# Kernel optimization log

Measured on AMD Instinct MI355X. Metric: run time of the kernel, lower is better.

## Reference

```python
import jax, jax.numpy as jnp
import numpy as np

N_NODES = 50000
N_EDGES = 800000
F_IN = 64
F_HID = 64
K = 3


def _cheb_norm(edge_index, edge_weight, n):
    # PyG ChebConv sym normalization with lambda_max=2: Lhat = -D^{-1/2} A D^{-1/2}
    # (diagonal of Lhat is exactly 0, so self-loop terms vanish)
    row, col = edge_index[0], edge_index[1]
    deg = jax.ops.segment_sum(edge_weight, row, num_segments=n)
    dis = jnp.where(deg > 0, jax.lax.rsqrt(jnp.where(deg > 0, deg, 1.0)), 0.0)
    return -dis[row] * edge_weight * dis[col]


def _prop(x, row, col, norm, n):
    # out[i] = sum_{e: col[e]=i} norm[e] * x[row[e]]
    return jax.ops.segment_sum(x[row] * norm[:, None], col, num_segments=n)


def _cheb_conv(x, W, b, row, col, norm, n):
    # ChebConv K=3: Tx0=x, Tx1=Lhat x, Tx2=2 Lhat Tx1 - Tx0
    tx0 = x
    tx1 = _prop(x, row, col, norm, n)
    tx2 = 2.0 * _prop(tx1, row, col, norm, n) - tx0
    return tx0 @ W[0] + tx1 @ W[1] + tx2 @ W[2] + b


def setup_inputs() -> dict:
    key = jax.random.key(0)
    ks = jax.random.split(key, 20)
    inp = {
        "x": jax.random.normal(ks[0], (N_NODES, F_IN), dtype=jnp.float32),
        "edge_index": jax.random.randint(ks[1], (2, N_EDGES), 0, N_NODES, dtype=jnp.int32),
        "edge_weight": jax.random.uniform(ks[2], (N_EDGES,), dtype=jnp.float32),
    }
    # 6 ChebConvs: x->gate (F_IN->F_HID) and h->gate (F_HID->F_HID) for z, r, h
    names_in = [("Wxz", "bxz", F_IN), ("Whz", "bhz", F_HID), ("Wxr", "bxr", F_IN),
                ("Whr", "bhr", F_HID), ("Wxh", "bxh", F_IN), ("Whh", "bhh", F_HID)]
    for i, (wn, bn, fin) in enumerate(names_in):
        scale = 1.0 / np.sqrt(fin)
        inp[wn] = jax.random.normal(ks[3 + i], (K, fin, F_HID), dtype=jnp.float32) * scale
        inp[bn] = jnp.zeros((F_HID,), dtype=jnp.float32)
    inp["Wlin"] = jax.random.normal(ks[12], (F_HID, 2), dtype=jnp.float32) * (1.0 / np.sqrt(F_HID))
    inp["blin"] = jnp.zeros((2,), dtype=jnp.float32)
    return inp


def reference(x, edge_index, edge_weight, Wxz, bxz, Whz, bhz, Wxr, bxr, Whr, bhr,
              Wxh, bxh, Whh, bhh, Wlin, blin):
    n = x.shape[0]
    row, col = edge_index[0], edge_index[1]
    norm = _cheb_norm(edge_index, edge_weight, n)
    h0 = jnp.zeros((n, F_HID), dtype=x.dtype)
    # GConvGRU single step (initial hidden state = 0)
    z = jax.nn.sigmoid(_cheb_conv(x, Wxz, bxz, row, col, norm, n)
                       + _cheb_conv(h0, Whz, bhz, row, col, norm, n))
    r = jax.nn.sigmoid(_cheb_conv(x, Wxr, bxr, row, col, norm, n)
                       + _cheb_conv(h0, Whr, bhr, row, col, norm, n))
    h_tilde = jnp.tanh(_cheb_conv(x, Wxh, bxh, row, col, norm, n)
                       + _cheb_conv(h0 * r, Whh, bhh, row, col, norm, n))
    h = z * h0 + (1.0 - z) * h_tilde
    # head: dropout in eval mode (identity) -> tanh -> linear -> sigmoid
    return jax.nn.sigmoid(jnp.tanh(h) @ Wlin + blin)
```

## Files before the change

kernel.cpp:

```cpp
#include <hip/hip_runtime.h>
#include <hip/hip_bf16.h>

#define N_NODES 50000
#define N_EDGES 800000
#define NB1 400
#define CH  2000
#define NBKT 196
#define CAP 8192
#define SORT_MAX 6144

typedef unsigned short ushort_t;
typedef unsigned long long u64;
typedef __attribute__((ext_vector_type(8))) short bf16x8;
typedef __attribute__((ext_vector_type(4))) float f32x4;

constexpr int GCUR_O  = 0;
constexpr int DIS_O   = 512;
constexpr int OFF_O   = 50512;
constexpr int CSLOT_O = 100544;
constexpr int RSLOT_O = 3311808;
constexpr int RW_O    = 4917440;
constexpr int ABUF_O  = 6517440;
constexpr int PBUF_O  = 11317440;
constexpr int XS_O    = 11329728;
constexpr int T1S_O   = RSLOT_O;

__device__ __forceinline__ ushort_t f32_to_bf16(float f) {
    unsigned u = __float_as_uint(f);
    u += 0x7fffu + ((u >> 16) & 1u);
    return (ushort_t)(u >> 16);
}
__device__ __forceinline__ float bflo(unsigned u) { return __uint_as_float(u << 16); }
__device__ __forceinline__ float bfhi(unsigned u) { return __uint_as_float(u & 0xffff0000u); }
__device__ __forceinline__ unsigned packbf2(float a, float b) {
    return (unsigned)f32_to_bf16(a) | ((unsigned)f32_to_bf16(b) << 16);
}
__device__ __forceinline__ float fsigmoid(float x) { return 1.f / (1.f + __expf(-x)); }
__device__ __forceinline__ float ftanh(float x) {
    x = fminf(15.f, fmaxf(-15.f, x));
    float e = __expf(2.f * x);
    return (e - 1.f) / (e + 1.f);
}

__global__ __launch_bounds__(512) void k1(
    const int* __restrict__ ei, const float* __restrict__ ew,
    const float* __restrict__ x, const float* __restrict__ Wxz,
    const float* __restrict__ Wxh, unsigned* __restrict__ gcur,
    u64* __restrict__ cslot, unsigned* __restrict__ rslot,
    unsigned* __restrict__ abuf, ushort_t* __restrict__ pbuf) {
    int bid = blockIdx.x, t = threadIdx.x;
    if (bid < NB1) {
        __shared__ unsigned colbuf[CH], rowbuf[CH];
        __shared__ unsigned hc[256], hr[256], bc[256], br[256];
        if (t < 256) { hc[t] = 0; hr[t] = 0; }
        __syncthreads();
        int e0 = bid * CH;
        for (int i = t; i < CH; i += 512) {
            unsigned r = (unsigned)ei[e0 + i];
            unsigned c = (unsigned)ei[N_EDGES + e0 + i];
            rowbuf[i] = r;
            colbuf[i] = c;
            atomicAdd(&hc[c >> 8], 1u);
            atomicAdd(&hr[r >> 8], 1u);
        }
        __syncthreads();
        if (t < NBKT) {
            bc[t] = atomicAdd(&gcur[t], hc[t]);
            br[t] = atomicAdd(&gcur[256 + t], hr[t]);
        }
        __syncthreads();
        if (t < 256) { hc[t] = 0; hr[t] = 0; }
        __syncthreads();
        for (int i = t; i < CH; i += 512) {
            unsigned c = colbuf[i];
            unsigned r = rowbuf[i];
            unsigned w = __float_as_uint(ew[e0 + i]);
            unsigned dc = c >> 8;
            unsigned pc = bc[dc] + atomicAdd(&hc[dc], 1u);
            if (pc < CAP)
                cslot[dc * CAP + pc] = ((u64)w << 32) | ((c & 255u) << 16) | (r & 0xFFFFu);
            unsigned dr = r >> 8;
            unsigned pr = br[dr] + atomicAdd(&hr[dr], 1u);
            if (pr < CAP) rslot[dr * CAP + pr] = (w & 0xFFFFFF00u) | (r & 255u);
        }
    } else if (bid < NB1 + 98) {
        int n0 = (bid - NB1) * 512;
        for (int idx = t; idx < 512 * 32; idx += 512) {
            int n = n0 + (idx >> 5);
            if (n < N_NODES) {
                int q = idx & 31;
                float2 xv = ((const float2*)x)[n * 32 + q];
                abuf[n * 96 + q] = packbf2(xv.x, xv.y);
            }
        }
    } else {
        for (int idx = t; idx < 24576; idx += 512) {
            int k = idx >> 7, n = idx & 127;
            float v = (n < 64) ? Wxz[k * 64 + n] : Wxh[k * 64 + (n - 64)];
            int c = n >> 4, s = k >> 5, l = (((k >> 3) & 3) << 4) | (n & 15), j = k & 7;
            pbuf[((c * 6 + s) * 64 + l) * 8 + j] = f32_to_bf16(v);
        }
    }
}

__global__ __launch_bounds__(512) void k2(
    const float* __restrict__ x, const unsigned* __restrict__ gcur,
    const u64* __restrict__ cslot, const unsigned* __restrict__ rslot,
    float* __restrict__ dis, int* __restrict__ off,
    u64* __restrict__ rw, unsigned* __restrict__ xs) {
    int bid = blockIdx.x, t = threadIdx.x;
    __shared__ unsigned rawA[SORT_MAX], rawB[SORT_MAX];
    __shared__ unsigned hist[256], hsc[256], cur[256], gs[256];
    __shared__ float facc[256];

    if (bid < NBKT) {
        if (t < 256) {
            gs[t] = (t < NBKT) ? gcur[t] : 0u;
            hist[t] = 0;
        }
        __syncthreads();
        for (int o = 1; o < 256; o <<= 1) {
            unsigned v = (t < 256 && t >= o) ? gs[t - o] : 0u;
            __syncthreads();
            if (t < 256) gs[t] += v;
            __syncthreads();
        }
        unsigned szb = gcur[bid];
        unsigned sz = min(szb, (unsigned)SORT_MAX);
        unsigned base = gs[bid] - szb;
        for (unsigned i = t; i < sz; i += 512) {
            u64 v = cslot[bid * CAP + i];
            unsigned lo = (unsigned)v;
            rawA[i] = lo;
            rawB[i] = (unsigned)(v >> 32);
            atomicAdd(&hist[(lo >> 16) & 255u], 1u);
        }
        __syncthreads();
        unsigned h0 = (t < 256) ? hist[t] : 0u;
        if (t < 256) hsc[t] = h0;
        __syncthreads();
        for (int o = 1; o < 256; o <<= 1) {
            unsigned v = (t < 256 && t >= o) ? hsc[t - o] : 0u;
            __syncthreads();
            if (t < 256) hsc[t] += v;
            __syncthreads();
        }
        if (t < 256) {
            hsc[t] -= h0;
            cur[t] = 0u;
            int c = bid * 256 + t;
            if (c <= N_NODES) off[c] = (int)(base + hsc[t]);
        }
        __syncthreads();
        for (unsigned i = t; i < sz; i += 512) {
            unsigned lo = rawA[i];
            unsigned d = (lo >> 16) & 255u;
            unsigned p = hsc[d] + atomicAdd(&cur[d], 1u);
            rw[base + p] = ((u64)rawB[i] << 32) | (lo & 0xFFFFu);
        }
    } else {
        int b = bid - NBKT;
        if (t < 256) facc[t] = 0.f;
        __syncthreads();
        unsigned szr = min(gcur[256 + b], (unsigned)CAP);
        for (unsigned i = t; i < szr; i += 512) {
            unsigned v = rslot[b * CAP + i];
            atomicAdd(&facc[v & 255u], __uint_as_float(v & 0xFFFFFF00u));
        }
        __syncthreads();
        if (t < 256) {
            float d = facc[t];
            float r = d > 0.f ? rsqrtf(d) : 0.f;
            facc[t] = r;
            int n = b * 256 + t;
            if (n < N_NODES) dis[n] = r;
        }
        __syncthreads();
        for (int idx = t; idx < 8192; idx += 512) {
            int nl = idx >> 5, q = idx & 31;
            int n = b * 256 + nl;
            if (n < N_NODES) {
                float2 xv = ((const float2*)x)[n * 32 + q];
                float r = facc[nl];
                xs[n * 32 + q] = packbf2(r * xv.x, r * xv.y);
            }
        }
    }
}

__global__ __launch_bounds__(256) void k_prop(
    const int* __restrict__ off, const u64* __restrict__ rw,
    const unsigned* __restrict__ xsrc, const float* __restrict__ dis,
    const float* __restrict__ xf, unsigned* __restrict__ abuf,
    unsigned* __restrict__ t1s, int mode) {
    int node = (blockIdx.x * 256 + threadIdx.x) >> 6;
    if (node >= N_NODES) return;
    int lane = threadIdx.x & 63, h = lane >> 5, q = lane & 31;
    int b = off[node], end = off[node + 1];
    float di = dis[node];
    float acc0 = 0.f, acc1 = 0.f;
    for (; b + 7 < end; b += 8) {
        u64 v0 = rw[b + h], v1 = rw[b + h + 2], v2 = rw[b + h + 4], v3 = rw[b + h + 6];
        unsigned r0 = (unsigned)v0 & 0xFFFFu, r1 = (unsigned)v1 & 0xFFFFu;
        unsigned r2 = (unsigned)v2 & 0xFFFFu, r3 = (unsigned)v3 & 0xFFFFu;
        float a0 = __uint_as_float((unsigned)(v0 >> 32));
        float a1 = __uint_as_float((unsigned)(v1 >> 32));
        float a2 = __uint_as_float((unsigned)(v2 >> 32));
        float a3 = __uint_as_float((unsigned)(v3 >> 32));
        unsigned u0 = xsrc[r0 * 32 + q], u1 = xsrc[r1 * 32 + q];
        unsigned u2 = xsrc[r2 * 32 + q], u3 = xsrc[r3 * 32 + q];
        acc0 += a0 * bflo(u0) + a1 * bflo(u1) + a2 * bflo(u2) + a3 * bflo(u3);
        acc1 += a0 * bfhi(u0) + a1 * bfhi(u1) + a2 * bfhi(u2) + a3 * bfhi(u3);
    }
    for (; b + 1 < end; b += 2) {
        u64 v = rw[b + h];
        unsigned r = (unsigned)v & 0xFFFFu;
        float a = __uint_as_float((unsigned)(v >> 32));
        unsigned u = xsrc[r * 32 + q];
        acc0 += a * bflo(u); acc1 += a * bfhi(u);
    }
    if (b < end && h == 0) {
        u64 v = rw[b];
        unsigned r = (unsigned)v & 0xFFFFu;
        float a = __uint_as_float((unsigned)(v >> 32));
        unsigned u = xsrc[r * 32 + q];
        acc0 += a * bflo(u); acc1 += a * bfhi(u);
    }
    acc0 += __shfl_xor(acc0, 32, 64);
    acc1 += __shfl_xor(acc1, 32, 64);
    if (h == 0) {
        float t0 = -di * acc0, t1v = -di * acc1;
        if (mode == 0) {
            abuf[node * 96 + 32 + q] = packbf2(t0, t1v);
            t1s[node * 32 + q] = packbf2(di * t0, di * t1v);
        } else {
            float2 xv = ((const float2*)xf)[node * 32 + q];
            abuf[node * 96 + 64 + q] = packbf2(2.f * t0 - xv.x, 2.f * t1v - xv.y);
        }
    }
}

__global__ __launch_bounds__(256) void k_gemm(
    const ushort_t* __restrict__ ab, const ushort_t* __restrict__ pbuf,
    const float* __restrict__ bxz, const float* __restrict__ bhz,
    const float* __restrict__ bxh, const float* __restrict__ bhh,
    const float* __restrict__ Wlin, const float* __restrict__ blin,
    float2* __restrict__ out) {
    __shared__ ushort_t bsh[24576];
    int tid = threadIdx.x;
    {
        uint4* s4 = (uint4*)bsh;
        const uint4* g4 = (const uint4*)pbuf;
        for (int i = tid; i < 3072; i += 256) s4[i] = g4[i];
    }
    __syncthreads();

    int wave = tid >> 6, lane = tid & 63;
    int quad = lane >> 4, m = lane & 15;
    int arow = blockIdx.x * 64 + wave * 16 + m;
    const ushort_t* ap = ab + (size_t)arow * 192 + quad * 8;

    f32x4 acc[8];
#pragma unroll
    for (int c = 0; c < 8; ++c) acc[c] = (f32x4){0.f, 0.f, 0.f, 0.f};
#pragma unroll
    for (int s = 0; s < 6; ++s) {
        bf16x8 af = *(const bf16x8*)(ap + s * 32);
#pragma unroll
        for (int c = 0; c < 8; ++c) {
            bf16x8 bfr = *(const bf16x8*)(bsh + ((c * 6 + s) * 64 + lane) * 8);
            acc[c] = __builtin_amdgcn_mfma_f32_16x16x32_bf16(af, bfr, acc[c], 0, 0, 0);
        }
    }
    float bzv[4], bhv[4], wl0[4], wl1[4];
#pragma unroll
    for (int c = 0; c < 4; ++c) {
        int col = c * 16 + m;
        bzv[c] = bxz[col] + bhz[col];
        bhv[c] = bxh[col] + bhh[col];
        wl0[c] = Wlin[2 * col];
        wl1[c] = Wlin[2 * col + 1];
    }
    float bl0 = blin[0], bl1 = blin[1];
#pragma unroll
    for (int i = 0; i < 4; ++i) {
        float p0 = 0.f, p1 = 0.f;
#pragma unroll
        for (int c = 0; c < 4; ++c) {
            float z  = fsigmoid(acc[c][i] + bzv[c]);
            float ht = ftanh(acc[c + 4][i] + bhv[c]);
            float t  = ftanh((1.f - z) * ht);
            p0 += t * wl0[c];
            p1 += t * wl1[c];
        }
        for (int o = 1; o <= 8; o <<= 1) {
            p0 += __shfl_xor(p0, o, 64);
            p1 += __shfl_xor(p1, o, 64);
        }
        int g = blockIdx.x * 64 + wave * 16 + quad * 4 + i;
        if (m == 0 && g < N_NODES)
            out[g] = make_float2(fsigmoid(p0 + bl0), fsigmoid(p1 + bl1));
    }
}

extern "C" void kernel_launch(void* const* d_in, const int* in_sizes, int n_in,
                              void* d_out, int out_size, void* d_ws, size_t ws_size,
                              hipStream_t stream) {
    const float* x    = (const float*)d_in[0];
    const int*   ei   = (const int*)d_in[1];
    const float* ew   = (const float*)d_in[2];
    const float* Wxz  = (const float*)d_in[3];
    const float* bxz  = (const float*)d_in[4];
    const float* bhz  = (const float*)d_in[6];
    const float* Wxh  = (const float*)d_in[11];
    const float* bxh  = (const float*)d_in[12];
    const float* bhh  = (const float*)d_in[14];
    const float* Wlin = (const float*)d_in[15];
    const float* blin = (const float*)d_in[16];

    float*    ws    = (float*)d_ws;
    unsigned* gcur  = (unsigned*)(ws + GCUR_O);
    float*    dis   = ws + DIS_O;
    int*      off   = (int*)(ws + OFF_O);
    u64*      cslot = (u64*)(ws + CSLOT_O);
    unsigned* rslot = (unsigned*)(ws + RSLOT_O);
    u64*      rw    = (u64*)(ws + RW_O);
    unsigned* abuf  = (unsigned*)(ws + ABUF_O);
    ushort_t* pbuf  = (ushort_t*)(ws + PBUF_O);
    unsigned* xs    = (unsigned*)(ws + XS_O);
    unsigned* t1s   = (unsigned*)(ws + T1S_O);

    hipMemsetAsync(d_ws, 0, 512 * 4, stream);

    k1<<<NB1 + 98 + 1, 512, 0, stream>>>(ei, ew, x, Wxz, Wxh, gcur, cslot, rslot, abuf, pbuf);
    k2<<<NBKT * 2, 512, 0, stream>>>(x, gcur, cslot, rslot, dis, off, rw, xs);
    k_prop<<<12500, 256, 0, stream>>>(off, rw, xs, dis, x, abuf, t1s, 0);
    k_prop<<<12500, 256, 0, stream>>>(off, rw, t1s, dis, x, abuf, abuf, 1);
    k_gemm<<<782, 256, 0, stream>>>((const ushort_t*)abuf, pbuf, bxz, bhz, bxh, bhh,
                                    Wlin, blin, (float2*)d_out);
}
```

Measured before the change: 214.2 us.

## Fuse x bf16 conversion into k2, use shuffle scans, and double gemm tiles per block

Moves the bf16 conversion of x into abuf from k1 into k2's per-bucket loop that already reads x, removing a separate pass over x. Replaces the LDS Hillis-Steele scans in k2 with a wave-shuffle based block scan to cut barriers. Reorders gather loads in k_prop and makes k_gemm process two 64-row tiles per block so the shared weight staging is amortised. Halving gemm blocks reduces parallelism somewhat.

```diff
diff --git a/kernel.cpp b/kernel.cpp
--- a/kernel.cpp
+++ b/kernel.cpp
@@ -42,12 +42,32 @@
     return (e - 1.f) / (e + 1.f);
 }
 
+__device__ __forceinline__ unsigned block_scan256_incl(unsigned v, int t, unsigned* wsum) {
+    int lane = t & 63;
+    unsigned sc = v;
+#pragma unroll
+    for (int o = 1; o < 64; o <<= 1) {
+        unsigned u = __shfl_up(sc, o, 64);
+        if (lane >= o) sc += u;
+    }
+    if (t < 256 && lane == 63) wsum[t >> 6] = sc;
+    __syncthreads();
+    if (t < 256) {
+        int wid = t >> 6;
+        unsigned off = 0;
+#pragma unroll
+        for (int wv = 0; wv < 3; ++wv) if (wv < wid) off += wsum[wv];
+        sc += off;
+    }
+    __syncthreads();
+    return sc;
+}
+
 __global__ __launch_bounds__(512) void k1(
     const int* __restrict__ ei, const float* __restrict__ ew,
-    const float* __restrict__ x, const float* __restrict__ Wxz,
-    const float* __restrict__ Wxh, unsigned* __restrict__ gcur,
-    u64* __restrict__ cslot, unsigned* __restrict__ rslot,
-    unsigned* __restrict__ abuf, ushort_t* __restrict__ pbuf) {
+    const float* __restrict__ Wxz, const float* __restrict__ Wxh,
+    unsigned* __restrict__ gcur, u64* __restrict__ cslot,
+    unsigned* __restrict__ rslot, ushort_t* __restrict__ pbuf) {
     int bid = blockIdx.x, t = threadIdx.x;
     if (bid < NB1) {
         __shared__ unsigned colbuf[CH], rowbuf[CH];
@@ -78,20 +98,10 @@
             unsigned dc = c >> 8;
             unsigned pc = bc[dc] + atomicAdd(&hc[dc], 1u);
             if (pc < CAP)
-                cslot[dc * CAP + pc] = ((u64)w << 32) | ((c & 255u) << 16) | (r & 0xFFFFu);
+                cslot[(size_t)dc * CAP + pc] = ((u64)w << 32) | ((c & 255u) << 16) | (r & 0xFFFFu);
             unsigned dr = r >> 8;
             unsigned pr = br[dr] + atomicAdd(&hr[dr], 1u);
-            if (pr < CAP) rslot[dr * CAP + pr] = (w & 0xFFFFFF00u) | (r & 255u);
-        }
-    } else if (bid < NB1 + 98) {
-        int n0 = (bid - NB1) * 512;
-        for (int idx = t; idx < 512 * 32; idx += 512) {
-            int n = n0 + (idx >> 5);
-            if (n < N_NODES) {
-                int q = idx & 31;
-                float2 xv = ((const float2*)x)[n * 32 + q];
-                abuf[n * 96 + q] = packbf2(xv.x, xv.y);
-            }
+            if (pr < CAP) rslot[(size_t)dr * CAP + pr] = (w & 0xFFFFFF00u) | (r & 255u);
         }
     } else {
         for (int idx = t; idx < 24576; idx += 512) {
@@ -106,30 +116,25 @@
 __global__ __launch_bounds__(512) void k2(
     const float* __restrict__ x, const unsigned* __restrict__ gcur,
     const u64* __restrict__ cslot, const unsigned* __restrict__ rslot,
-    float* __restrict__ dis, int* __restrict__ off,
-    u64* __restrict__ rw, unsigned* __restrict__ xs) {
+    float* __restrict__ dis, int* __restrict__ off, u64* __restrict__ rw,
+    unsigned* __restrict__ abuf, unsigned* __restrict__ xs) {
     int bid = blockIdx.x, t = threadIdx.x;
     __shared__ unsigned rawA[SORT_MAX], rawB[SORT_MAX];
     __shared__ unsigned hist[256], hsc[256], cur[256], gs[256];
+    __shared__ unsigned wsum[8];
     __shared__ float facc[256];
 
     if (bid < NBKT) {
-        if (t < 256) {
-            gs[t] = (t < NBKT) ? gcur[t] : 0u;
-            hist[t] = 0;
-        }
-        __syncthreads();
-        for (int o = 1; o < 256; o <<= 1) {
-            unsigned v = (t < 256 && t >= o) ? gs[t - o] : 0u;
-            __syncthreads();
-            if (t < 256) gs[t] += v;
-            __syncthreads();
-        }
+        unsigned szv = (t < NBKT) ? gcur[t] : 0u;
+        unsigned inc = block_scan256_incl(szv, t, wsum);
+        if (t < 256) gs[t] = inc - szv;
+        if (t < 256) hist[t] = 0;
+        __syncthreads();
         unsigned szb = gcur[bid];
         unsigned sz = min(szb, (unsigned)SORT_MAX);
-        unsigned base = gs[bid] - szb;
+        unsigned base = gs[bid];
         for (unsigned i = t; i < sz; i += 512) {
-            u64 v = cslot[bid * CAP + i];
+            u64 v = cslot[(size_t)bid * CAP + i];
             unsigned lo = (unsigned)v;
             rawA[i] = lo;
             rawB[i] = (unsigned)(v >> 32);
@@ -137,16 +142,9 @@
         }
         __syncthreads();
         unsigned h0 = (t < 256) ? hist[t] : 0u;
-        if (t < 256) hsc[t] = h0;
-        __syncthreads();
-        for (int o = 1; o < 256; o <<= 1) {
-            unsigned v = (t < 256 && t >= o) ? hsc[t - o] : 0u;
-            __syncthreads();
-            if (t < 256) hsc[t] += v;
-            __syncthreads();
-        }
+        unsigned hinc = block_scan256_incl(h0, t, wsum);
         if (t < 256) {
-            hsc[t] -= h0;
+            hsc[t] = hinc - h0;
             cur[t] = 0u;
             int c = bid * 256 + t;
             if (c <= N_NODES) off[c] = (int)(base + hsc[t]);
@@ -163,10 +161,9 @@
         if (t < 256) facc[t] = 0.f;
         __syncthreads();
         unsigned szr = min(gcur[256 + b], (unsigned)CAP);
-        for (unsigned i = t; i < szr; i += 512) {
-            unsigned v = rslot[b * CAP + i];
-            atomicAdd(&facc[v & 255u], __uint_as_float(v & 0xFFFFFF00u));
-        }
+        const unsigned* rs = rslot + (size_t)b * CAP;
+        for (unsigned i = t; i < szr; i += 512)
+            atomicAdd(&facc[rs[i] & 255u], __uint_as_float(rs[i] & 0xFFFFFF00u));
         __syncthreads();
         if (t < 256) {
             float d = facc[t];
@@ -182,6 +179,7 @@
             if (n < N_NODES) {
                 float2 xv = ((const float2*)x)[n * 32 + q];
                 float r = facc[nl];
+                abuf[n * 96 + q] = packbf2(xv.x, xv.y);
                 xs[n * 32 + q] = packbf2(r * xv.x, r * xv.y);
             }
         }
@@ -201,29 +199,27 @@
     float acc0 = 0.f, acc1 = 0.f;
     for (; b + 7 < end; b += 8) {
         u64 v0 = rw[b + h], v1 = rw[b + h + 2], v2 = rw[b + h + 4], v3 = rw[b + h + 6];
-        unsigned r0 = (unsigned)v0 & 0xFFFFu, r1 = (unsigned)v1 & 0xFFFFu;
-        unsigned r2 = (unsigned)v2 & 0xFFFFu, r3 = (unsigned)v3 & 0xFFFFu;
+        unsigned u0 = xsrc[((unsigned)v0 & 0xFFFFu) * 32 + q];
+        unsigned u1 = xsrc[((unsigned)v1 & 0xFFFFu) * 32 + q];
+        unsigned u2 = xsrc[((unsigned)v2 & 0xFFFFu) * 32 + q];
+        unsigned u3 = xsrc[((unsigned)v3 & 0xFFFFu) * 32 + q];
         float a0 = __uint_as_float((unsigned)(v0 >> 32));
         float a1 = __uint_as_float((unsigned)(v1 >> 32));
         float a2 = __uint_as_float((unsigned)(v2 >> 32));
         float a3 = __uint_as_float((unsigned)(v3 >> 32));
-        unsigned u0 = xsrc[r0 * 32 + q], u1 = xsrc[r1 * 32 + q];
-        unsigned u2 = xsrc[r2 * 32 + q], u3 = xsrc[r3 * 32 + q];
         acc0 += a0 * bflo(u0) + a1 * bflo(u1) + a2 * bflo(u2) + a3 * bflo(u3);
         acc1 += a0 * bfhi(u0) + a1 * bfhi(u1) + a2 * bfhi(u2) + a3 * bfhi(u3);
     }
     for (; b + 1 < end; b += 2) {
         u64 v = rw[b + h];
-        unsigned r = (unsigned)v & 0xFFFFu;
+        unsigned u = xsrc[((unsigned)v & 0xFFFFu) * 32 + q];
         float a = __uint_as_float((unsigned)(v >> 32));
-        unsigned u = xsrc[r * 32 + q];
         acc0 += a * bflo(u); acc1 += a * bfhi(u);
     }
     if (b < end && h == 0) {
         u64 v = rw[b];
-        unsigned r = (unsigned)v & 0xFFFFu;
+        unsigned u = xsrc[((unsigned)v & 0xFFFFu) * 32 + q];
         float a = __uint_as_float((unsigned)(v >> 32));
-        unsigned u = xsrc[r * 32 + q];
         acc0 += a * bflo(u); acc1 += a * bfhi(u);
     }
     acc0 += __shfl_xor(acc0, 32, 64);
@@ -257,21 +253,7 @@
 
     int wave = tid >> 6, lane = tid & 63;
     int quad = lane >> 4, m = lane & 15;
-    int arow = blockIdx.x * 64 + wave * 16 + m;
-    const ushort_t* ap = ab + (size_t)arow * 192 + quad * 8;
-
-    f32x4 acc[8];
-#pragma unroll
-    for (int c = 0; c < 8; ++c) acc[c] = (f32x4){0.f, 0.f, 0.f, 0.f};
-#pragma unroll
-    for (int s = 0; s < 6; ++s) {
-        bf16x8 af = *(const bf16x8*)(ap + s * 32);
-#pragma unroll
-        for (int c = 0; c < 8; ++c) {
-            bf16x8 bfr = *(const bf16x8*)(bsh + ((c * 6 + s) * 64 + lane) * 8);
-            acc[c] = __builtin_amdgcn_mfma_f32_16x16x32_bf16(af, bfr, acc[c], 0, 0, 0);
-        }
-    }
+
     float bzv[4], bhv[4], wl0[4], wl1[4];
 #pragma unroll
     for (int c = 0; c < 4; ++c) {
@@ -282,24 +264,43 @@
         wl1[c] = Wlin[2 * col + 1];
     }
     float bl0 = blin[0], bl1 = blin[1];
-#pragma unroll
-    for (int i = 0; i < 4; ++i) {
-        float p0 = 0.f, p1 = 0.f;
-#pragma unroll
-        for (int c = 0; c < 4; ++c) {
-            float z  = fsigmoid(acc[c][i] + bzv[c]);
-            float ht = ftanh(acc[c + 4][i] + bhv[c]);
-            float t  = ftanh((1.f - z) * ht);
-            p0 += t * wl0[c];
-            p1 += t * wl1[c];
-        }
-        for (int o = 1; o <= 8; o <<= 1) {
-            p0 += __shfl_xor(p0, o, 64);
-            p1 += __shfl_xor(p1, o, 64);
-        }
-        int g = blockIdx.x * 64 + wave * 16 + quad * 4 + i;
-        if (m == 0 && g < N_NODES)
-            out[g] = make_float2(fsigmoid(p0 + bl0), fsigmoid(p1 + bl1));
+
+    for (int tile = 0; tile < 2; ++tile) {
+        int n0 = (blockIdx.x * 2 + tile) * 64;
+        int arow = n0 + wave * 16 + m;
+        const ushort_t* ap = ab + (size_t)arow * 192 + quad * 8;
+
+        f32x4 acc[8];
+#pragma unroll
+        for (int c = 0; c < 8; ++c) acc[c] = (f32x4){0.f, 0.f, 0.f, 0.f};
+#pragma unroll
+        for (int s = 0; s < 6; ++s) {
+            bf16x8 af = *(const bf16x8*)(ap + s * 32);
+#pragma unroll
+            for (int c = 0; c < 8; ++c) {
+                bf16x8 bfr = *(const bf16x8*)(bsh + ((c * 6 + s) * 64 + lane) * 8);
+                acc[c] = __builtin_amdgcn_mfma_f32_16x16x32_bf16(af, bfr, acc[c], 0, 0, 0);
+            }
+        }
+#pragma unroll
+        for (int i = 0; i < 4; ++i) {
+            float p0 = 0.f, p1 = 0.f;
+#pragma unroll
+            for (int c = 0; c < 4; ++c) {
+                float z  = fsigmoid(acc[c][i] + bzv[c]);
+                float ht = ftanh(acc[c + 4][i] + bhv[c]);
+                float t  = ftanh((1.f - z) * ht);
+                p0 += t * wl0[c];
+                p1 += t * wl1[c];
+            }
+            for (int o = 1; o <= 8; o <<= 1) {
+                p0 += __shfl_xor(p0, o, 64);
+                p1 += __shfl_xor(p1, o, 64);
+            }
+            int g = n0 + wave * 16 + quad * 4 + i;
+            if (m == 0 && g < N_NODES)
+                out[g] = make_float2(fsigmoid(p0 + bl0), fsigmoid(p1 + bl1));
+        }
     }
 }
 
@@ -332,10 +333,10 @@
 
     hipMemsetAsync(d_ws, 0, 512 * 4, stream);
 
-    k1<<<NB1 + 98 + 1, 512, 0, stream>>>(ei, ew, x, Wxz, Wxh, gcur, cslot, rslot, abuf, pbuf);
-    k2<<<NBKT * 2, 512, 0, stream>>>(x, gcur, cslot, rslot, dis, off, rw, xs);
+    k1<<<NB1 + 1, 512, 0, stream>>>(ei, ew, Wxz, Wxh, gcur, cslot, rslot, pbuf);
+    k2<<<NBKT * 2, 512, 0, stream>>>(x, gcur, cslot, rslot, dis, off, rw, abuf, xs);
     k_prop<<<12500, 256, 0, stream>>>(off, rw, xs, dis, x, abuf, t1s, 0);
     k_prop<<<12500, 256, 0, stream>>>(off, rw, t1s, dis, x, abuf, abuf, 1);
-    k_gemm<<<782, 256, 0, stream>>>((const ushort_t*)abuf, pbuf, bxz, bhz, bxh, bhh,
+    k_gemm<<<391, 256, 0, stream>>>((const ushort_t*)abuf, pbuf, bxz, bhz, bxh, bhh,
                                     Wlin, blin, (float2*)d_out);
 }
```

Result: no change. 216.3 us (+1.0%).
